# Kernel optimization log

Measured on AMD Instinct MI355X. Metric: run time of the kernel, lower is better.

The kernel has to match this reference:

```python
import jax, jax.numpy as jnp
import numpy as np
from jax import lax

T, B, I, H = 512, 128, 256, 1024


def setup_inputs() -> dict:
    key = jax.random.key(0)
    ks = jax.random.split(key, 7)
    s_ih = 1.0 / np.sqrt(H)
    return {
        "inputs": jax.random.normal(ks[0], (T, B, I), dtype=jnp.float32),
        "h0": jax.random.normal(ks[1], (B, H), dtype=jnp.float32),
        "c0": jax.random.normal(ks[2], (B, H), dtype=jnp.float32),
        "W_ih": jax.random.uniform(ks[3], (4 * H, I), dtype=jnp.float32, minval=-s_ih, maxval=s_ih),
        "W_hh": jax.random.uniform(ks[4], (4 * H, H), dtype=jnp.float32, minval=-s_ih, maxval=s_ih),
        "b_ih": jax.random.uniform(ks[5], (4 * H,), dtype=jnp.float32, minval=-s_ih, maxval=s_ih),
        "b_hh": jax.random.uniform(ks[6], (4 * H,), dtype=jnp.float32, minval=-s_ih, maxval=s_ih),
    }


def reference(inputs, h0, c0, W_ih, W_hh, b_ih, b_hh):
    # Precompute input projections for all timesteps in one big GEMM.
    # [T, B, 4H]
    x_proj = jnp.einsum('tbi,gi->tbg', inputs, W_ih) + b_ih + b_hh
    hidden = W_hh.shape[1]

    def step(carry, xp):
        h, c = carry
        gates = xp + h @ W_hh.T  # [B, 4H]
        i_g, f_g, g_g, o_g = jnp.split(gates, 4, axis=-1)
        i_g = jax.nn.sigmoid(i_g)
        f_g = jax.nn.sigmoid(f_g)
        g_g = jnp.tanh(g_g)
        o_g = jax.nn.sigmoid(o_g)
        c_new = f_g * c + i_g * g_g
        h_new = o_g * jnp.tanh(c_new)
        return (h_new, c_new), h_new

    (h_final, c_final), outputs = lax.scan(step, (h0, c0), x_proj)
    # outputs: [T, B, H]; matches torch stack over dim 0 (batch_first=False)
    return outputs, h_final, c_final
```

## Files before the change

### kernel.cpp

```cpp
#include <hip/hip_runtime.h>


#define T_STEPS 512
#define BATCH   128
#define IN_DIM  256
#define HID     1024
#define GATES   4096
#define KDIM    1280

typedef __bf16 bf16x8 __attribute__((ext_vector_type(8)));
typedef float  f32x4  __attribute__((ext_vector_type(4)));

__device__ __forceinline__ unsigned short f2bf(float f) {
  unsigned int u = __builtin_bit_cast(unsigned int, f);
  unsigned int r = (u + 0x7FFFu + ((u >> 16) & 1u)) >> 16;
  return (unsigned short)r;
}

__global__ void cast_weights(const float* __restrict__ Wih,
                             const float* __restrict__ Whh,
                             unsigned short* __restrict__ Wbf) {
  int gid = blockIdx.x * blockDim.x + threadIdx.x;
  if (gid >= GATES * (KDIM / 4)) return;
  int n  = gid / (KDIM / 4);
  int k4 = (gid % (KDIM / 4)) * 4;
  float4 v;
  if (k4 < IN_DIM) v = *reinterpret_cast<const float4*>(Wih + (size_t)n * IN_DIM + k4);
  else             v = *reinterpret_cast<const float4*>(Whh + (size_t)n * HID + (k4 - IN_DIM));
  ushort4 o;
  o.x = f2bf(v.x); o.y = f2bf(v.y); o.z = f2bf(v.z); o.w = f2bf(v.w);
  *reinterpret_cast<ushort4*>(Wbf + (size_t)n * KDIM + k4) = o;
}

__global__ void init_state(const float* __restrict__ h0, const float* __restrict__ c0,
                           const float* __restrict__ bih, const float* __restrict__ bhh,
                           unsigned short* __restrict__ hbf0, float* __restrict__ cws,
                           float* __restrict__ bsum) {
  int i = blockIdx.x * blockDim.x + threadIdx.x;
  if (i < BATCH * HID) { hbf0[i] = f2bf(h0[i]); cws[i] = c0[i]; }
  if (i < GATES) bsum[i] = bih[i] + bhh[i];
}

__global__ __launch_bounds__(256) void lstm_step(
    const float* __restrict__ x_t,
    const unsigned short* __restrict__ Wbf,
    const float* __restrict__ bsum,
    const unsigned short* __restrict__ h_in,
    unsigned short* __restrict__ h_out,
    float* __restrict__ c_ws,
    float* __restrict__ out_t)
{
  __shared__ __align__(16) unsigned short As[64][72];
  __shared__ __align__(16) unsigned short Bs[32][72];
  __shared__ __align__(16) float Gs[64][36];

  const int tid  = threadIdx.x;
  const int cg   = blockIdx.x;
  const int rg   = blockIdx.y;
  const int row0 = rg * 64;
  const int j0   = cg * 8;

  const int wave = tid >> 6;
  const int lane = tid & 63;
  const int col  = lane & 15;
  const int quad = lane >> 4;
  const int mrow = wave * 16 + col;

  f32x4 acc0 = {0.f, 0.f, 0.f, 0.f};
  f32x4 acc1 = {0.f, 0.f, 0.f, 0.f};

  const int wrow = tid >> 3;
  const int kcB  = tid & 7;
  const int gB = wrow >> 3, jjB = wrow & 7;
  const unsigned short* wsrc =
      Wbf + (size_t)(gB * HID + j0 + jjB) * KDIM + kcB * 8;

  for (int kt = 0; kt < KDIM / 64; ++kt) {
    const int kbase = kt * 64;
    #pragma unroll
    for (int p = 0; p < 2; ++p) {
      int idx = p * 256 + tid;
      int row = idx >> 3;
      int kc  = idx & 7;
      int k   = kbase + kc * 8;
      if (k < IN_DIM) {
        const float* src = x_t + (size_t)(row0 + row) * IN_DIM + k;
        float4 f0 = *reinterpret_cast<const float4*>(src);
        float4 f1 = *reinterpret_cast<const float4*>(src + 4);
        ushort4 u0, u1;
        u0.x = f2bf(f0.x); u0.y = f2bf(f0.y); u0.z = f2bf(f0.z); u0.w = f2bf(f0.w);
        u1.x = f2bf(f1.x); u1.y = f2bf(f1.y); u1.z = f2bf(f1.z); u1.w = f2bf(f1.w);
        *reinterpret_cast<ushort4*>(&As[row][kc * 8])     = u0;
        *reinterpret_cast<ushort4*>(&As[row][kc * 8 + 4]) = u1;
      } else {
        const unsigned short* src = h_in + (size_t)(row0 + row) * HID + (k - IN_DIM);
        *reinterpret_cast<uint4*>(&As[row][kc * 8]) =
            *reinterpret_cast<const uint4*>(src);
      }
    }
    *reinterpret_cast<uint4*>(&Bs[wrow][kcB * 8]) =
        *reinterpret_cast<const uint4*>(wsrc + kbase);
    __syncthreads();

    #pragma unroll
    for (int s = 0; s < 2; ++s) {
      bf16x8 a  = *reinterpret_cast<const bf16x8*>(&As[mrow][s * 32 + quad * 8]);
      bf16x8 b0 = *reinterpret_cast<const bf16x8*>(&Bs[col][s * 32 + quad * 8]);
      bf16x8 b1 = *reinterpret_cast<const bf16x8*>(&Bs[16 + col][s * 32 + quad * 8]);
      acc0 = __builtin_amdgcn_mfma_f32_16x16x32_bf16(a, b0, acc0, 0, 0, 0);
      acc1 = __builtin_amdgcn_mfma_f32_16x16x32_bf16(a, b1, acc1, 0, 0, 0);
    }
    __syncthreads();
  }

  #pragma unroll
  for (int r = 0; r < 4; ++r) {
    Gs[wave * 16 + quad * 4 + r][col]      = acc0[r];
    Gs[wave * 16 + quad * 4 + r][16 + col] = acc1[r];
  }
  __syncthreads();

  #pragma unroll
  for (int p = 0; p < 2; ++p) {
    int idx = p * 256 + tid;
    int row = idx >> 3;
    int jj  = idx & 7;
    float ig = Gs[row][jj]      + bsum[j0 + jj];
    float fg = Gs[row][8 + jj]  + bsum[HID + j0 + jj];
    float gg = Gs[row][16 + jj] + bsum[2 * HID + j0 + jj];
    float og = Gs[row][24 + jj] + bsum[3 * HID + j0 + jj];
    ig = 1.f / (1.f + __expf(-ig));
    fg = 1.f / (1.f + __expf(-fg));
    og = 1.f / (1.f + __expf(-og));
    gg = tanhf(gg);
    int b = row0 + row;
    int j = j0 + jj;
    size_t off = (size_t)b * HID + j;
    float c_old = c_ws[off];
    float c_new = fg * c_old + ig * gg;
    float h     = og * tanhf(c_new);
    c_ws[off]  = c_new;
    out_t[off] = h;
    h_out[off] = f2bf(h);
  }
}

__global__ void finalize(const float* __restrict__ c_ws, float* __restrict__ out) {
  int i = blockIdx.x * blockDim.x + threadIdx.x;
  if (i < BATCH * HID) {
    const size_t base = (size_t)T_STEPS * BATCH * HID;
    out[base + i] = out[(size_t)(T_STEPS - 1) * BATCH * HID + i];
    out[base + BATCH * HID + i] = c_ws[i];
  }
}

extern "C" void kernel_launch(void* const* d_in, const int* in_sizes, int n_in,
                              void* d_out, int out_size, void* d_ws, size_t ws_size,
                              hipStream_t stream) {
  const float* x   = (const float*)d_in[0];
  const float* h0  = (const float*)d_in[1];
  const float* c0  = (const float*)d_in[2];
  const float* Wih = (const float*)d_in[3];
  const float* Whh = (const float*)d_in[4];
  const float* bih = (const float*)d_in[5];
  const float* bhh = (const float*)d_in[6];
  float* out = (float*)d_out;

  char* ws = (char*)d_ws;
  unsigned short* Wbf  = (unsigned short*)ws;
  float*          bsum = (float*)(ws + 10485760);
  unsigned short* hbf  = (unsigned short*)(ws + 10485760 + 16384);
  float*          cws  = (float*)(ws + 10485760 + 16384 + 524288);

  cast_weights<<<dim3((GATES * (KDIM / 4) + 255) / 256), 256, 0, stream>>>(Wih, Whh, Wbf);
  init_state<<<dim3((BATCH * HID + 255) / 256), 256, 0, stream>>>(h0, c0, bih, bhh,
                                                                  hbf, cws, bsum);
  for (int t = 0; t < T_STEPS; ++t) {
    lstm_step<<<dim3(128, 2), 256, 0, stream>>>(
        x + (size_t)t * BATCH * IN_DIM, Wbf, bsum,
        hbf + (size_t)(t & 1) * BATCH * HID,
        hbf + (size_t)((t + 1) & 1) * BATCH * HID,
        cws, out + (size_t)t * BATCH * HID);
  }
  finalize<<<dim3((BATCH * HID + 255) / 256), 256, 0, stream>>>(cws, out);
}
```

Baseline: 9.181 ms.

## Replace per-timestep launches with persistent cooperative LSTM kernel holding weights in LDS

Replaces the 512 per-step kernel launches with one cooperative persistent kernel of 256 blocks that syncs the whole grid between timesteps. Each block casts its slice of W_ih/W_hh to bf16 once and keeps it in LDS, so weights are not re-read from global memory every step. The cell state stays in registers, and the input and h tiles are double-buffered with register prefetch. Clamped exp-based sigmoid/tanh replace tanhf. The cost is a grid-wide barrier per step and a dependence on all blocks being co-resident with about 110KB of LDS each.

Result: slower. 21.19 ms (+130.8%).

```diff
diff --git a/kernel.cpp b/kernel.cpp
--- a/kernel.cpp
+++ b/kernel.cpp
@@ -1,12 +1,21 @@
 #include <hip/hip_runtime.h>
+#include <hip/hip_cooperative_groups.h>
+
+namespace cg = cooperative_groups;
 
 
 #define T_STEPS 512
 #define BATCH   128
 #define IN_DIM  256
 #define HID     1024
-#define GATES   4096
 #define KDIM    1280
+#define NK      20
+#define NKX     4
+
+#define WS_OFF  0
+#define AS_OFF  82432
+#define GS_OFF  100864
+#define LDS_BYTES 110080
 
 typedef __bf16 bf16x8 __attribute__((ext_vector_type(8)));
 typedef float  f32x4  __attribute__((ext_vector_type(4)));
@@ -17,141 +26,203 @@
   return (unsigned short)r;
 }
 
-__global__ void cast_weights(const float* __restrict__ Wih,
-                             const float* __restrict__ Whh,
-                             unsigned short* __restrict__ Wbf) {
-  int gid = blockIdx.x * blockDim.x + threadIdx.x;
-  if (gid >= GATES * (KDIM / 4)) return;
-  int n  = gid / (KDIM / 4);
-  int k4 = (gid % (KDIM / 4)) * 4;
-  float4 v;
-  if (k4 < IN_DIM) v = *reinterpret_cast<const float4*>(Wih + (size_t)n * IN_DIM + k4);
-  else             v = *reinterpret_cast<const float4*>(Whh + (size_t)n * HID + (k4 - IN_DIM));
-  ushort4 o;
-  o.x = f2bf(v.x); o.y = f2bf(v.y); o.z = f2bf(v.z); o.w = f2bf(v.w);
-  *reinterpret_cast<ushort4*>(Wbf + (size_t)n * KDIM + k4) = o;
-}
-
-__global__ void init_state(const float* __restrict__ h0, const float* __restrict__ c0,
-                           const float* __restrict__ bih, const float* __restrict__ bhh,
-                           unsigned short* __restrict__ hbf0, float* __restrict__ cws,
-                           float* __restrict__ bsum) {
-  int i = blockIdx.x * blockDim.x + threadIdx.x;
-  if (i < BATCH * HID) { hbf0[i] = f2bf(h0[i]); cws[i] = c0[i]; }
-  if (i < GATES) bsum[i] = bih[i] + bhh[i];
-}
-
-__global__ __launch_bounds__(256) void lstm_step(
-    const float* __restrict__ x_t,
-    const unsigned short* __restrict__ Wbf,
-    const float* __restrict__ bsum,
-    const unsigned short* __restrict__ h_in,
-    unsigned short* __restrict__ h_out,
-    float* __restrict__ c_ws,
-    float* __restrict__ out_t)
+__device__ __forceinline__ float sigmoid_fast(float v) {
+  v = fminf(fmaxf(v, -30.f), 30.f);
+  return 1.f / (1.f + __expf(-v));
+}
+
+__device__ __forceinline__ float tanh_fast(float v) {
+  v = fminf(fmaxf(v, -15.f), 15.f);
+  float e = __expf(-2.f * v);
+  return (1.f - e) / (1.f + e);
+}
+
+__global__ __launch_bounds__(512, 1) void lstm_persistent(
+    const float* __restrict__ x,
+    const float* __restrict__ h0,
+    const float* __restrict__ c0,
+    const float* __restrict__ Wih,
+    const float* __restrict__ Whh,
+    const float* __restrict__ bih,
+    const float* __restrict__ bhh,
+    unsigned short* __restrict__ hb,
+    float* __restrict__ out)
 {
-  __shared__ __align__(16) unsigned short As[64][72];
-  __shared__ __align__(16) unsigned short Bs[32][72];
-  __shared__ __align__(16) float Gs[64][36];
+  extern __shared__ char smem[];
+  unsigned short (*Ws)[1288]     = (unsigned short(*)[1288])(smem + WS_OFF);
+  unsigned short (*As)[64][72]   = (unsigned short(*)[64][72])(smem + AS_OFF);
+  float (*Gs)[36]                = (float(*)[36])(smem + GS_OFF);
 
   const int tid  = threadIdx.x;
-  const int cg   = blockIdx.x;
-  const int rg   = blockIdx.y;
+  const int bx   = blockIdx.x;
+  const int cgi  = bx & 127;
+  const int rg   = bx >> 7;
   const int row0 = rg * 64;
-  const int j0   = cg * 8;
+  const int j0   = cgi * 8;
 
   const int wave = tid >> 6;
   const int lane = tid & 63;
   const int col  = lane & 15;
   const int quad = lane >> 4;
-  const int mrow = wave * 16 + col;
-
-  f32x4 acc0 = {0.f, 0.f, 0.f, 0.f};
-  f32x4 acc1 = {0.f, 0.f, 0.f, 0.f};
-
-  const int wrow = tid >> 3;
-  const int kcB  = tid & 7;
-  const int gB = wrow >> 3, jjB = wrow & 7;
-  const unsigned short* wsrc =
-      Wbf + (size_t)(gB * HID + j0 + jjB) * KDIM + kcB * 8;
-
-  for (int kt = 0; kt < KDIM / 64; ++kt) {
-    const int kbase = kt * 64;
+  const int mrow = (wave & 3) * 16 + col;
+  const int nsel = wave >> 2;
+  const int brow = nsel * 16 + col;
+
+  {
+    const int w   = tid >> 4;
+    const int t16 = tid & 15;
+    const int g = w >> 3, jj = w & 7;
+    const size_t grow = (size_t)g * HID + j0 + jj;
+    const float* wih_r = Wih + grow * IN_DIM;
+    const float* whh_r = Whh + grow * HID;
     #pragma unroll
-    for (int p = 0; p < 2; ++p) {
-      int idx = p * 256 + tid;
-      int row = idx >> 3;
-      int kc  = idx & 7;
-      int k   = kbase + kc * 8;
-      if (k < IN_DIM) {
-        const float* src = x_t + (size_t)(row0 + row) * IN_DIM + k;
-        float4 f0 = *reinterpret_cast<const float4*>(src);
-        float4 f1 = *reinterpret_cast<const float4*>(src + 4);
-        ushort4 u0, u1;
-        u0.x = f2bf(f0.x); u0.y = f2bf(f0.y); u0.z = f2bf(f0.z); u0.w = f2bf(f0.w);
-        u1.x = f2bf(f1.x); u1.y = f2bf(f1.y); u1.z = f2bf(f1.z); u1.w = f2bf(f1.w);
-        *reinterpret_cast<ushort4*>(&As[row][kc * 8])     = u0;
-        *reinterpret_cast<ushort4*>(&As[row][kc * 8 + 4]) = u1;
-      } else {
-        const unsigned short* src = h_in + (size_t)(row0 + row) * HID + (k - IN_DIM);
-        *reinterpret_cast<uint4*>(&As[row][kc * 8]) =
-            *reinterpret_cast<const uint4*>(src);
+    for (int c = 0; c < 10; ++c) {
+      int k = t16 * 80 + c * 8;
+      const float* src = (k < IN_DIM) ? (wih_r + k) : (whh_r + (k - IN_DIM));
+      float4 f0 = *reinterpret_cast<const float4*>(src);
+      float4 f1 = *reinterpret_cast<const float4*>(src + 4);
+      ushort4 u0, u1;
+      u0.x = f2bf(f0.x); u0.y = f2bf(f0.y); u0.z = f2bf(f0.z); u0.w = f2bf(f0.w);
+      u1.x = f2bf(f1.x); u1.y = f2bf(f1.y); u1.z = f2bf(f1.z); u1.w = f2bf(f1.w);
+      *reinterpret_cast<ushort4*>(&Ws[w][k])     = u0;
+      *reinterpret_cast<ushort4*>(&Ws[w][k + 4]) = u1;
+    }
+  }
+
+  const int erow = tid >> 3;
+  const int ejj  = tid & 7;
+  const size_t eoff = (size_t)(row0 + erow) * HID + (j0 + ejj);
+  float c_reg = c0[eoff];
+  const float bi = bih[j0 + ejj]           + bhh[j0 + ejj];
+  const float bf_ = bih[HID + j0 + ejj]    + bhh[HID + j0 + ejj];
+  const float bg = bih[2 * HID + j0 + ejj] + bhh[2 * HID + j0 + ejj];
+  const float bo = bih[3 * HID + j0 + ejj] + bhh[3 * HID + j0 + ejj];
+  hb[eoff] = f2bf(h0[eoff]);
+
+  const int srow = tid >> 3;
+  const int skc  = tid & 7;
+  const float* xbase = x + (size_t)(row0 + srow) * IN_DIM + skc * 8;
+
+  float4 fa0, fb0, fa1, fb1;
+  uint4  u0v = {0,0,0,0}, u1v = {0,0,0,0};
+
+  {
+    const float* xt = xbase;
+    fa0 = *reinterpret_cast<const float4*>(xt);
+    fb0 = *reinterpret_cast<const float4*>(xt + 4);
+    fa1 = *reinterpret_cast<const float4*>(xt + 64);
+    fb1 = *reinterpret_cast<const float4*>(xt + 64 + 4);
+  }
+
+  cg::this_grid().sync();
+
+  float h_last = 0.f;
+
+  for (int t = 0; t < T_STEPS; ++t) {
+    const float* xt = xbase + (size_t)t * BATCH * IN_DIM;
+    const unsigned short* hin =
+        hb + (size_t)(t & 1) * (BATCH * HID) + (size_t)(row0 + srow) * HID + skc * 8;
+
+    {
+      unsigned short* dst = &As[0][srow][skc * 8];
+      ushort4 a, b;
+      a.x = f2bf(fa0.x); a.y = f2bf(fa0.y); a.z = f2bf(fa0.z); a.w = f2bf(fa0.w);
+      b.x = f2bf(fb0.x); b.y = f2bf(fb0.y); b.z = f2bf(fb0.z); b.w = f2bf(fb0.w);
+      *reinterpret_cast<ushort4*>(dst)     = a;
+      *reinterpret_cast<ushort4*>(dst + 4) = b;
+    }
+    __syncthreads();
+
+    f32x4 acc = {0.f, 0.f, 0.f, 0.f};
+
+    #pragma unroll 2
+    for (int kt = 0; kt < NK; ++kt) {
+      const bool even = ((kt & 1) == 0);
+      if (kt + 2 < NK) {
+        const int ki = kt + 2;
+        if (even) {
+          if (ki < NKX) {
+            fa0 = *reinterpret_cast<const float4*>(xt + ki * 64);
+            fb0 = *reinterpret_cast<const float4*>(xt + ki * 64 + 4);
+          } else {
+            u0v = *reinterpret_cast<const uint4*>(hin + (ki - NKX) * 64);
+          }
+        } else {
+          if (ki < NKX) {
+            fa1 = *reinterpret_cast<const float4*>(xt + ki * 64);
+            fb1 = *reinterpret_cast<const float4*>(xt + ki * 64 + 4);
+          } else {
+            u1v = *reinterpret_cast<const uint4*>(hin + (ki - NKX) * 64);
+          }
+        }
       }
-    }
-    *reinterpret_cast<uint4*>(&Bs[wrow][kcB * 8]) =
-        *reinterpret_cast<const uint4*>(wsrc + kbase);
+      #pragma unroll
+      for (int s = 0; s < 2; ++s) {
+        bf16x8 a = *reinterpret_cast<const bf16x8*>(&As[kt & 1][mrow][s * 32 + quad * 8]);
+        bf16x8 b = *reinterpret_cast<const bf16x8*>(&Ws[brow][kt * 64 + s * 32 + quad * 8]);
+        acc = __builtin_amdgcn_mfma_f32_16x16x32_bf16(a, b, acc, 0, 0, 0);
+      }
+      if (kt + 1 < NK) {
+        const int kc = kt + 1;
+        unsigned short* dst = &As[kc & 1][srow][skc * 8];
+        if (even) {
+          if (kc < NKX) {
+            ushort4 a, b;
+            a.x = f2bf(fa1.x); a.y = f2bf(fa1.y); a.z = f2bf(fa1.z); a.w = f2bf(fa1.w);
+            b.x = f2bf(fb1.x); b.y = f2bf(fb1.y); b.z = f2bf(fb1.z); b.w = f2bf(fb1.w);
+            *reinterpret_cast<ushort4*>(dst)     = a;
+            *reinterpret_cast<ushort4*>(dst + 4) = b;
+          } else {
+            *reinterpret_cast<uint4*>(dst) = u1v;
+          }
+        } else {
+          if (kc < NKX) {
+            ushort4 a, b;
+            a.x = f2bf(fa0.x); a.y = f2bf(fa0.y); a.z = f2bf(fa0.z); a.w = f2bf(fa0.w);
+            b.x = f2bf(fb0.x); b.y = f2bf(fb0.y); b.z = f2bf(fb0.z); b.w = f2bf(fb0.w);
+            *reinterpret_cast<ushort4*>(dst)     = a;
+            *reinterpret_cast<ushort4*>(dst + 4) = b;
+          } else {
+            *reinterpret_cast<uint4*>(dst) = u0v;
+          }
+        }
+      }
+      __syncthreads();
+    }
+
+    #pragma unroll
+    for (int r = 0; r < 4; ++r)
+      Gs[(wave & 3) * 16 + quad * 4 + r][nsel * 16 + col] = acc[r];
     __syncthreads();
 
-    #pragma unroll
-    for (int s = 0; s < 2; ++s) {
-      bf16x8 a  = *reinterpret_cast<const bf16x8*>(&As[mrow][s * 32 + quad * 8]);
-      bf16x8 b0 = *reinterpret_cast<const bf16x8*>(&Bs[col][s * 32 + quad * 8]);
-      bf16x8 b1 = *reinterpret_cast<const bf16x8*>(&Bs[16 + col][s * 32 + quad * 8]);
-      acc0 = __builtin_amdgcn_mfma_f32_16x16x32_bf16(a, b0, acc0, 0, 0, 0);
-      acc1 = __builtin_amdgcn_mfma_f32_16x16x32_bf16(a, b1, acc1, 0, 0, 0);
-    }
-    __syncthreads();
+    float ig = Gs[erow][ejj]      + bi;
+    float fg = Gs[erow][8 + ejj]  + bf_;
+    float gg = Gs[erow][16 + ejj] + bg;
+    float og = Gs[erow][24 + ejj] + bo;
+    ig = sigmoid_fast(ig);
+    fg = sigmoid_fast(fg);
+    og = sigmoid_fast(og);
+    gg = tanh_fast(gg);
+    c_reg = fg * c_reg + ig * gg;
+    float hval = og * tanh_fast(c_reg);
+    out[(size_t)t * BATCH * HID + eoff] = hval;
+    hb[(size_t)((t + 1) & 1) * (BATCH * HID) + eoff] = f2bf(hval);
+    h_last = hval;
+
+    if (t + 1 < T_STEPS) {
+      const float* xn = xbase + (size_t)(t + 1) * BATCH * IN_DIM;
+      fa0 = *reinterpret_cast<const float4*>(xn);
+      fb0 = *reinterpret_cast<const float4*>(xn + 4);
+      fa1 = *reinterpret_cast<const float4*>(xn + 64);
+      fb1 = *reinterpret_cast<const float4*>(xn + 64 + 4);
+    }
+
+    cg::this_grid().sync();
   }
 
-  #pragma unroll
-  for (int r = 0; r < 4; ++r) {
-    Gs[wave * 16 + quad * 4 + r][col]      = acc0[r];
-    Gs[wave * 16 + quad * 4 + r][16 + col] = acc1[r];
-  }
-  __syncthreads();
-
-  #pragma unroll
-  for (int p = 0; p < 2; ++p) {
-    int idx = p * 256 + tid;
-    int row = idx >> 3;
-    int jj  = idx & 7;
-    float ig = Gs[row][jj]      + bsum[j0 + jj];
-    float fg = Gs[row][8 + jj]  + bsum[HID + j0 + jj];
-    float gg = Gs[row][16 + jj] + bsum[2 * HID + j0 + jj];
-    float og = Gs[row][24 + jj] + bsum[3 * HID + j0 + jj];
-    ig = 1.f / (1.f + __expf(-ig));
-    fg = 1.f / (1.f + __expf(-fg));
-    og = 1.f / (1.f + __expf(-og));
-    gg = tanhf(gg);
-    int b = row0 + row;
-    int j = j0 + jj;
-    size_t off = (size_t)b * HID + j;
-    float c_old = c_ws[off];
-    float c_new = fg * c_old + ig * gg;
-    float h     = og * tanhf(c_new);
-    c_ws[off]  = c_new;
-    out_t[off] = h;
-    h_out[off] = f2bf(h);
-  }
-}
-
-__global__ void finalize(const float* __restrict__ c_ws, float* __restrict__ out) {
-  int i = blockIdx.x * blockDim.x + threadIdx.x;
-  if (i < BATCH * HID) {
-    const size_t base = (size_t)T_STEPS * BATCH * HID;
-    out[base + i] = out[(size_t)(T_STEPS - 1) * BATCH * HID + i];
-    out[base + BATCH * HID + i] = c_ws[i];
-  }
+  const size_t fin = (size_t)T_STEPS * BATCH * HID;
+  out[fin + eoff] = h_last;
+  out[fin + BATCH * HID + eoff] = c_reg;
 }
 
 extern "C" void kernel_launch(void* const* d_in, const int* in_sizes, int n_in,
@@ -165,22 +236,13 @@
   const float* bih = (const float*)d_in[5];
   const float* bhh = (const float*)d_in[6];
   float* out = (float*)d_out;
-
-  char* ws = (char*)d_ws;
-  unsigned short* Wbf  = (unsigned short*)ws;
-  float*          bsum = (float*)(ws + 10485760);
-  unsigned short* hbf  = (unsigned short*)(ws + 10485760 + 16384);
-  float*          cws  = (float*)(ws + 10485760 + 16384 + 524288);
-
-  cast_weights<<<dim3((GATES * (KDIM / 4) + 255) / 256), 256, 0, stream>>>(Wih, Whh, Wbf);
-  init_state<<<dim3((BATCH * HID + 255) / 256), 256, 0, stream>>>(h0, c0, bih, bhh,
-                                                                  hbf, cws, bsum);
-  for (int t = 0; t < T_STEPS; ++t) {
-    lstm_step<<<dim3(128, 2), 256, 0, stream>>>(
-        x + (size_t)t * BATCH * IN_DIM, Wbf, bsum,
-        hbf + (size_t)(t & 1) * BATCH * HID,
-        hbf + (size_t)((t + 1) & 1) * BATCH * HID,
-        cws, out + (size_t)t * BATCH * HID);
-  }
-  finalize<<<dim3((BATCH * HID + 255) / 256), 256, 0, stream>>>(cws, out);
-}
+  unsigned short* hb = (unsigned short*)d_ws;
+
+  hipFuncSetAttribute((const void*)lstm_persistent,
+                      hipFuncAttributeMaxDynamicSharedMemorySize, LDS_BYTES);
+
+  void* args[] = {(void*)&x, (void*)&h0, (void*)&c0, (void*)&Wih, (void*)&Whh,
+                  (void*)&bih, (void*)&bhh, (void*)&hb, (void*)&out};
+  hipLaunchCooperativeKernel((void*)lstm_persistent, dim3(256), dim3(512),
+                             args, LDS_BYTES, stream);
+}
```
